# Kernel optimization log

Measured on AMD Instinct MI355X. Metric: run time of the kernel, lower is better.

Reference implementation:

```python
import jax, jax.numpy as jnp
import numpy as np

N, E = 50000, 400000
IN_DIM, EDGE_F, OUT_DIM, EDGE_OUT, H = 256, 64, 32, 64, 8
ALPHA, TEMP, EPS = 0.2, 1.0, 1e-5


def lrelu(x):
    return jax.nn.leaky_relu(x, negative_slope=ALPHA)


def batch_norm(x, gamma, beta):
    # torch BatchNorm1d training-mode: biased variance over the batch dim
    mu = x.mean(0)
    var = x.var(0)
    return (x - mu) * jax.lax.rsqrt(var + EPS) * gamma + beta


def setup_inputs() -> dict:
    key = jax.random.key(0)
    ks = jax.random.split(key, 16)
    s = 0.05
    return {
        "node_inputs": jax.random.normal(ks[0], (N, IN_DIM), jnp.float32),
        "edge_inputs": jax.random.normal(ks[1], (E, EDGE_F), jnp.float32),
        "fc_w": jax.random.normal(ks[2], (IN_DIM, H * OUT_DIM), jnp.float32) * s,
        "attn_l": jax.random.normal(ks[3], (H, OUT_DIM), jnp.float32) * s,
        "attn_r": jax.random.normal(ks[4], (H, OUT_DIM), jnp.float32) * s,
        "ae_w1": jax.random.normal(ks[5], (EDGE_F, OUT_DIM), jnp.float32) * s,
        "ae_b1": jnp.zeros((OUT_DIM,), jnp.float32),
        "ae_w2": jax.random.normal(ks[6], (OUT_DIM, H), jnp.float32) * s,
        "ae_b2": jnp.zeros((H,), jnp.float32),
        "bn_n_g": jnp.ones((H * OUT_DIM,), jnp.float32),
        "bn_n_b": jnp.zeros((H * OUT_DIM,), jnp.float32),
        "eu_node_w": jax.random.normal(ks[7], (2 * H * OUT_DIM, EDGE_OUT), jnp.float32) * s,
        "eu_edge_w": jax.random.normal(ks[8], (EDGE_F, EDGE_OUT), jnp.float32) * s,
        "eu_final_w": jax.random.normal(ks[9], (2 * EDGE_OUT, EDGE_OUT), jnp.float32) * s,
        "bn_e_g": jnp.ones((EDGE_OUT,), jnp.float32),
        "bn_e_b": jnp.zeros((EDGE_OUT,), jnp.float32),
        "src": jax.random.randint(ks[10], (E,), 0, N, jnp.int32),
        "dst": jax.random.randint(ks[11], (E,), 0, N, jnp.int32),
    }


def reference(node_inputs, edge_inputs, fc_w, attn_l, attn_r, ae_w1, ae_b1, ae_w2,
              ae_b2, bn_n_g, bn_n_b, eu_node_w, eu_edge_w, eu_final_w, bn_e_g,
              bn_e_b, src, dst):
    # node projection, per-head attention scalars (dropout prob = 0 -> identity)
    ft = (node_inputs @ fc_w).reshape(N, H, OUT_DIM)          # [N,H,D]
    a1 = jnp.einsum('nhd,hd->nh', ft, attn_l)                 # [N,H]
    a2 = jnp.einsum('nhd,hd->nh', ft, attn_r)                 # [N,H]
    # edge-feature attention MLP: Linear -> LeakyReLU -> Linear
    e_attn = lrelu(edge_inputs @ ae_w1 + ae_b1) @ ae_w2 + ae_b2  # [E,H]
    a = lrelu(a1[src] + a2[dst] + e_attn) * TEMP              # [E,H]
    # two-pass edge softmax over incoming edges (segment by dst)
    a_max = jax.ops.segment_max(a, dst, num_segments=N)       # [N,H]
    a = jnp.exp(a - a_max[dst])                               # [E,H]
    z = jax.ops.segment_sum(a, dst, num_segments=N)           # [N,H]
    # weighted message aggregation
    msg = ft[src] * a[:, :, None]                             # [E,H,D]
    agg = jax.ops.segment_sum(msg, dst, num_segments=N)       # [N,H,D]
    z_safe = jnp.where(z == 0, 1.0, z)
    node_out = (agg / z_safe[:, :, None]).reshape(N, H * OUT_DIM)
    node_out = node_out + node_inputs                         # residual (dims match)
    node_out = batch_norm(lrelu(node_out), bn_n_g, bn_n_b)
    # edge update MLP
    node_f = lrelu(jnp.concatenate([node_out[src], node_out[dst]], -1) @ eu_node_w)
    edge_f = lrelu(edge_inputs @ eu_edge_w)
    edge_out = jnp.concatenate([node_f, edge_f], -1) @ eu_final_w
    edge_out = edge_out + edge_inputs                         # residual (dims match)
    edge_out = batch_norm(lrelu(edge_out), bn_e_g, bn_e_b)
    return node_out, edge_out
```

## Files before the change

kernel.cpp:

```cpp
#include <hip/hip_runtime.h>
#include <hip/hip_bf16.h>

typedef __hip_bfloat16 bf16;

#define N_NODES 50000
#define N_EDGES 400000
#define IN_DIM  256
#define EDGE_F  64
#define OUT_DIM 32
#define EDGE_OUT 64
#define NHEADS  8
#define HD      256
#define ALPHA   0.2f
#define BN_EPS  1e-5f

#define NBINS 50432
#define NBLK  197

__device__ __forceinline__ float b2f(bf16 v){ return __bfloat162float(v); }
__device__ __forceinline__ bf16  f2b(float v){ return __float2bfloat16(v); }
__device__ __forceinline__ float lrelu(float x){ return x > 0.f ? x : ALPHA*x; }
__device__ __forceinline__ unsigned fenc(float f){ unsigned u=__float_as_uint(f); return (u&0x80000000u)? ~u : (u|0x80000000u); }
__device__ __forceinline__ float fdec(unsigned k){ return (k&0x80000000u)? __uint_as_float(k&0x7fffffffu) : __uint_as_float(~k); }

template<bool F32> __device__ __forceinline__ float LD(const void* p, long i){
  if constexpr (F32) return ((const float*)p)[i];
  else               return b2f(((const bf16*)p)[i]);
}
template<bool F32> __device__ __forceinline__ void ST(void* p, long i, float v){
  if constexpr (F32) ((float*)p)[i] = v;
  else               ((bf16*)p)[i] = f2b(v);
}
template<bool F32> __device__ __forceinline__ void* ESEC(void* out){
  return (char*)out + (size_t)N_NODES*HD*(F32?4:2);
}

typedef __attribute__((ext_vector_type(8))) short bf16x8;
typedef __attribute__((ext_vector_type(4))) float f32x4;

union PackU { uint4 u; bf16x8 v; };
__device__ __forceinline__ bf16x8 as_frag(uint4 w){ PackU p; p.u = w; return p.v; }
__device__ __forceinline__ bf16x8 zero_frag(){ PackU p; p.u = make_uint4(0,0,0,0); return p.v; }

#define MFMA16(a,b,c) __builtin_amdgcn_mfma_f32_16x16x32_bf16(a,b,c,0,0,0)

__device__ __forceinline__ void split8(float4 a, float4 b, bf16x8& hi, bf16x8& lo){
  float v[8] = {a.x,a.y,a.z,a.w,b.x,b.y,b.z,b.w};
  unsigned hu[4], lu[4];
  #pragma unroll
  for(int i=0;i<4;i++){
    unsigned u0 = __float_as_uint(v[2*i]);
    unsigned u1 = __float_as_uint(v[2*i+1]);
    unsigned h0 = u0 & 0xffff0000u, h1 = u1 & 0xffff0000u;
    hu[i] = (u0>>16) | h1;
    float l0 = v[2*i]   - __uint_as_float(h0);
    float l1 = v[2*i+1] - __uint_as_float(h1);
    union { bf16 h; unsigned short s; } c0, c1; c0.h = f2b(l0); c1.h = f2b(l1);
    lu[i] = (unsigned)c0.s | ((unsigned)c1.s << 16);
  }
  PackU H,L;
  H.u = make_uint4(hu[0],hu[1],hu[2],hu[3]);
  L.u = make_uint4(lu[0],lu[1],lu[2],lu[3]);
  hi = H.v; lo = L.v;
}

template<bool F32> __device__ __forceinline__ void load_split(const void* p, long off, bf16x8& hi, bf16x8& lo){
  if constexpr(F32){
    const float* f = (const float*)p + off;
    float4 a = *(const float4*)f;
    float4 b = *(const float4*)(f+4);
    split8(a,b,hi,lo);
  } else {
    hi = as_frag(*(const uint4*)((const bf16*)p + off));
    lo = zero_frag();
  }
}

__global__ __launch_bounds__(256) void k_detect(const unsigned short* __restrict__ u,
                                                int* __restrict__ flag){
  __shared__ int cnt;
  if(threadIdx.x==0) cnt=0;
  __syncthreads();
  int local=0;
  for(int i=threadIdx.x;i<8192;i+=256){
    int e = (u[i]>>7)&0xFF;
    if(e>=200) local++;
  }
  atomicAdd(&cnt, local);
  __syncthreads();
  if(threadIdx.x==0) *flag = (cnt>64) ? 1 : 0;
}

__global__ __launch_bounds__(256) void k_hist(const int* __restrict__ dst, int* __restrict__ cnt){
  int e = blockIdx.x*256 + threadIdx.x;
  if(e < N_EDGES){
    unsigned d = (unsigned)dst[e];
    if(d < N_NODES) atomicAdd(&cnt[d], 1);
  }
}
__global__ __launch_bounds__(256) void k_scan1(const int* __restrict__ cnt, int* __restrict__ rs,
                                               int* __restrict__ btot){
  __shared__ int s[256];
  int t = threadIdx.x; int i = blockIdx.x*256 + t;
  int v = cnt[i]; s[t] = v; __syncthreads();
  for(int off=1; off<256; off<<=1){
    int x = (t>=off) ? s[t-off] : 0; __syncthreads();
    s[t] += x; __syncthreads();
  }
  rs[i] = s[t] - v;
  if(t==255) btot[blockIdx.x] = s[t];
}
__global__ __launch_bounds__(256) void k_scan2(const int* __restrict__ btot, int* __restrict__ bsum){
  __shared__ int s[256];
  int t = threadIdx.x;
  int v = (t<NBLK) ? btot[t] : 0; s[t] = v; __syncthreads();
  for(int off=1; off<256; off<<=1){
    int x = (t>=off) ? s[t-off] : 0; __syncthreads();
    s[t] += x; __syncthreads();
  }
  if(t<NBLK) bsum[t] = s[t] - v;
}
__global__ __launch_bounds__(256) void k_scan3(int* __restrict__ rs, const int* __restrict__ bsum,
                                               int* __restrict__ cursor){
  int i = blockIdx.x*256 + threadIdx.x;
  int r = rs[i] + bsum[blockIdx.x];
  rs[i] = r; cursor[i] = r;
}

template<bool F32> __device__ void pack_body(const void* wn, const void* we, const void* wf,
                                             unsigned short* out){
  int i = blockIdx.x*256 + threadIdx.x;
  if(i >= 45056) return;
  const void* srcp; int idx;
  if(i < 32768){ srcp = wn; idx = i; }
  else if(i < 36864){ srcp = we; idx = i - 32768; }
  else { srcp = wf; idx = i - 36864; }
  int j = idx & 7, lane = (idx>>3)&63, nt = (idx>>9)&3, ks = idx>>11;
  int k = ks*32 + ((lane>>4)<<3) + j;
  int n = (nt<<4) + (lane&15);
  union { bf16 h; unsigned short s; } u;
  u.h = f2b(LD<F32>(srcp, (long)k*EDGE_OUT + n));
  out[i] = u.s;
}
__global__ __launch_bounds__(256) void k_pack_w(const void* wn, const void* we, const void* wf,
                                                unsigned short* out, const int* flag){
  if(*flag) pack_body<true >(wn,we,wf,out);
  else      pack_body<false>(wn,we,wf,out);
}
template<bool F32> __device__ void pack_fc_body(const void* w, unsigned short* out){
  int i = blockIdx.x*256 + threadIdx.x;
  int j = i&7, lane = (i>>3)&63, nt = (i>>9)&15, ks = i>>13;
  int k = ks*32 + ((lane>>4)<<3) + j;
  int n = (nt<<4) + (lane&15);
  union { bf16 h; unsigned short s; } u;
  u.h = f2b(LD<F32>(w, (long)k*HD + n));
  out[i] = u.s;
}
__global__ __launch_bounds__(256) void k_pack_fc(const void* w, unsigned short* out, const int* flag){
  if(*flag) pack_fc_body<true >(w,out);
  else      pack_fc_body<false>(w,out);
}

template<bool F32> __device__ void nproj_body(const void* x, const unsigned short* wpf, float* ft){
  const uint4* w4 = (const uint4*)wpf;
  int wid = threadIdx.x>>6, lane = threadIdx.x&63;
  int row16 = lane&15, kgrp = lane>>4;
  int r0 = blockIdx.x*64 + wid*16;
  long arow = r0 + row16; if(arow >= N_NODES) arow = N_NODES-1;
  f32x4 acc[16];
  #pragma unroll
  for(int nt=0;nt<16;nt++) acc[nt] = (f32x4){0.f,0.f,0.f,0.f};
  #pragma unroll 2
  for(int ks=0;ks<8;ks++){
    bf16x8 ah, al;
    load_split<F32>(x, arow*IN_DIM + ks*32 + kgrp*8, ah, al);
    const uint4* wb = w4 + (size_t)(ks*16)*64 + lane;
    #pragma unroll
    for(int nt=0;nt<16;nt++){
      bf16x8 b = as_frag(wb[nt*64]);
      if constexpr(F32) acc[nt] = MFMA16(al, b, acc[nt]);
      acc[nt] = MFMA16(ah, b, acc[nt]);
    }
  }
  #pragma unroll
  for(int nt=0;nt<16;nt++)
    #pragma unroll
    for(int j=0;j<4;j++){
      int r = r0 + kgrp*4 + j;
      if(r < N_NODES) ft[(long)r*HD + nt*16 + row16] = acc[nt][j];
    }
}
__global__ __launch_bounds__(256) void k_node_proj(const void* x, const unsigned short* wpf,
                                                   float* ft, const int* flag){
  if(*flag) nproj_body<true >(x,wpf,ft);
  else      nproj_body<false>(x,wpf,ft);
}

template<bool F32> __device__ void attn_body(const float* ft, const void* al, const void* ar,
                                             float* a1, float* a2){
  int gid = blockIdx.x*8 + (threadIdx.x>>5);
  int d   = threadIdx.x & 31;
  int h   = gid & 7;
  float v  = ft[(long)gid*OUT_DIM + d];
  float s1 = v * LD<F32>(al, h*OUT_DIM + d);
  float s2 = v * LD<F32>(ar, h*OUT_DIM + d);
  for(int o=16;o>0;o>>=1){ s1 += __shfl_down(s1,o,32); s2 += __shfl_down(s2,o,32); }
  if(d==0){ a1[gid]=s1; a2[gid]=s2; }
}
__global__ __launch_bounds__(256) void k_attn(const float* ft, const void* al, const void* ar,
                                              float* a1, float* a2, const int* flag){
  if(*flag) attn_body<true >(ft,al,ar,a1,a2);
  else      attn_body<false>(ft,al,ar,a1,a2);
}

template<bool F32> __device__ void edge_attn_body(const void* ein, const void* w1, const void* b1,
                                                  const void* w2, const void* b2,
                                                  const float* a1, const float* a2,
                                                  const int* src, const int* dst,
                                                  int* cursor, unsigned short* psrc,
                                                  float* a_edge, unsigned* amax, float* sm){
  float* sw1 = sm;
  float* sw2 = sw1 + 2048;
  float* sb1 = sw2 + 256;
  float* sb2 = sb1 + 32;
  float* se  = sb2 + 8;
  float* st  = se  + 512;
  int t = threadIdx.x;
  #pragma unroll
  for(int i=0;i<8;i++) sw1[i*256+t] = LD<F32>(w1, i*256+t);
  sw2[t] = LD<F32>(w2, t);
  if(t<OUT_DIM) sb1[t]=LD<F32>(b1,t);
  if(t<NHEADS)  sb2[t]=LD<F32>(b2,t);
  int e0 = blockIdx.x*8;
  #pragma unroll
  for(int i=0;i<2;i++){ int idx=i*256+t; se[idx] = LD<F32>(ein,(long)e0*EDGE_F + idx); }
  __syncthreads();
  int r = t>>5, j = t&31;
  float acc = sb1[j];
  #pragma unroll 4
  for(int k=0;k<EDGE_F;k++) acc += se[r*64+k]*sw1[k*OUT_DIM+j];
  st[r*32+j] = lrelu(acc);
  __syncthreads();
  if(t<64){
    int rr = t>>3, h = t&7;
    float s = sb2[h];
    #pragma unroll
    for(int jj=0;jj<OUT_DIM;jj++) s += st[rr*32+jj]*sw2[jj*NHEADS+h];
    int e = e0+rr;
    int sv = src[e], dv = dst[e];
    float av = lrelu(a1[sv*NHEADS+h] + a2[dv*NHEADS+h] + s);
    int pos = 0;
    if(h==0) pos = atomicAdd(&cursor[dv], 1);
    pos = __shfl(pos, rr*8, 64);
    a_edge[(long)pos*NHEADS + h] = av;
    if(h==0) psrc[pos] = (unsigned short)sv;
    atomicMax(&amax[dv*NHEADS+h], fenc(av));
  }
}
__global__ __launch_bounds__(256) void k_edge_attn(const void* ein, const void* w1, const void* b1,
                                                   const void* w2, const void* b2,
                                                   const float* a1, const float* a2,
                                                   const int* src, const int* dst,
                                                   int* cursor, unsigned short* psrc,
                                                   float* a_edge, unsigned* amax, const int* flag){
  extern __shared__ float smemf[];
  if(*flag) edge_attn_body<true >(ein,w1,b1,w2,b2,a1,a2,src,dst,cursor,psrc,a_edge,amax,smemf);
  else      edge_attn_body<false>(ein,w1,b1,w2,b2,a1,a2,src,dst,cursor,psrc,a_edge,amax,smemf);
}

template<bool F32> __device__ void agg_body(const int* rs, const unsigned short* psrc,
                                            const float* a_edge, const unsigned* amax,
                                            const float* ft, const void* xin, void* xout,
                                            double* dstats, double* sm){
  int wid = threadIdx.x>>6, lane = threadIdx.x&63;
  int gw = blockIdx.x*4 + wid, nw = gridDim.x*4;
  int h0 = lane>>5;
  double s4[4]={0,0,0,0}, q4[4]={0,0,0,0};
  for(int n=gw; n<N_NODES; n+=nw){
    int b0 = rs[n], b1 = rs[n+1];
    if(b1 > N_EDGES) b1 = N_EDGES;
    if(b0 > b1) b0 = b1;
    float m = (lane<8) ? fdec(amax[n*NHEADS+lane]) : 0.f;
    float zl = 0.f;
    float acc[4] = {0,0,0,0};
    for(int i=b0;i<b1;++i){
      float av = 0.f;
      if(lane<8){ av = __expf(a_edge[(long)i*NHEADS+lane] - m); zl += av; }
      int sv = psrc[i];
      const float* fr = ft + (long)sv*HD;
      #pragma unroll
      for(int q=0;q<4;q++){
        float a = __shfl(av, h0 + 2*q, 64);
        acc[q] = fmaf(a, fr[lane + 64*q], acc[q]);
      }
    }
    #pragma unroll
    for(int q=0;q<4;q++){
      float z = __shfl(zl, h0 + 2*q, 64);
      float zs = (z==0.f) ? 1.f : z;
      int c = lane + 64*q;
      float xv = lrelu(acc[q]/zs + LD<F32>(xin,(long)n*HD + c));
      ST<F32>(xout,(long)n*HD + c, xv);
      s4[q] += xv; q4[q] += (double)xv*(double)xv;
    }
  }
  double* ls = sm; double* lq = sm + 256;
  for(int w=0;w<4;w++){
    if(wid==w){
      #pragma unroll
      for(int q=0;q<4;q++){
        int c = lane + 64*q;
        if(w==0){ ls[c]=s4[q]; lq[c]=q4[q]; }
        else    { ls[c]+=s4[q]; lq[c]+=q4[q]; }
      }
    }
    __syncthreads();
  }
  int t = threadIdx.x;
  unsafeAtomicAdd(&dstats[t],    ls[t]);
  unsafeAtomicAdd(&dstats[HD+t], lq[t]);
}
__global__ __launch_bounds__(256) void k_agg(const int* rs, const unsigned short* psrc,
                                             const float* a_edge, const unsigned* amax,
                                             const float* ft, const void* xin, void* xout,
                                             double* dstats, const int* flag){
  extern __shared__ double smemd[];
  if(*flag) agg_body<true >(rs,psrc,a_edge,amax,ft,xin,xout,dstats,smemd);
  else      agg_body<false>(rs,psrc,a_edge,amax,ft,xin,xout,dstats,smemd);
}

template<bool F32> __device__ void bn_params_body(const double* dstats, const void* g,
                                                  const void* b, float* scsh, int C, double invM){
  int t = threadIdx.x;
  if(t>=C) return;
  double mu  = dstats[t]*invM;
  double var = dstats[C+t]*invM - mu*mu;
  if(var < 0.0) var = 0.0;
  float sc = LD<F32>(g,t) * rsqrtf((float)var + BN_EPS);
  scsh[t]   = sc;
  scsh[C+t] = LD<F32>(b,t) - (float)mu*sc;
}
__global__ void k_bn_params(const double* dstats, const void* g, const void* b,
                            float* scsh, int C, double invM, const int* flag){
  if(*flag) bn_params_body<true >(dstats,g,b,scsh,C,invM);
  else      bn_params_body<false>(dstats,g,b,scsh,C,invM);
}

template<bool F32> __device__ void node_apply_body(void* x, const float* scsh){
  int t = threadIdx.x;
  float sc = scsh[t], sh = scsh[HD+t];
  for(long i=(long)blockIdx.x*256+t; i<(long)N_NODES*HD; i+=(long)gridDim.x*256){
    ST<F32>(x, i, fmaf(LD<F32>(x,i), sc, sh));
  }
}
__global__ __launch_bounds__(256) void k_node_apply(void* x, const float* scsh, const int* flag){
  if(*flag) node_apply_body<true >(x,scsh);
  else      node_apply_body<false>(x,scsh);
}

template<bool F32> __device__ void pq_body(const void* nodeb, const unsigned short* wpack,
                                           float* P, float* Q){
  const uint4* wn4 = (const uint4*)wpack;
  int wid = threadIdx.x>>6, lane = threadIdx.x&63;
  int row16 = lane&15, kgrp = lane>>4;
  int r0 = blockIdx.x*64 + wid*16;
  long arow = r0 + row16; if(arow >= N_NODES) arow = N_NODES-1;
  f32x4 pacc[4], qacc[4];
  #pragma unroll
  for(int nt=0;nt<4;nt++){ pacc[nt]=(f32x4){0.f,0.f,0.f,0.f}; qacc[nt]=(f32x4){0.f,0.f,0.f,0.f}; }
  #pragma unroll 2
  for(int ks=0;ks<8;ks++){
    bf16x8 ah, al;
    load_split<F32>(nodeb, arow*HD + ks*32 + kgrp*8, ah, al);
    const uint4* wbP = wn4 + (size_t)(ks*4)*64 + lane;
    const uint4* wbQ = wn4 + (size_t)((8+ks)*4)*64 + lane;
    #pragma unroll
    for(int nt=0;nt<4;nt++){
      bf16x8 bP = as_frag(wbP[nt*64]);
      bf16x8 bQ = as_frag(wbQ[nt*64]);
      pacc[nt] = MFMA16(ah, bP, pacc[nt]);
      qacc[nt] = MFMA16(ah, bQ, qacc[nt]);
      if constexpr(F32){
        pacc[nt] = MFMA16(al, bP, pacc[nt]);
        qacc[nt] = MFMA16(al, bQ, qacc[nt]);
      }
    }
  }
  #pragma unroll
  for(int nt=0;nt<4;nt++)
    #pragma unroll
    for(int j=0;j<4;j++){
      int r = r0 + kgrp*4 + j;
      if(r < N_NODES){
        P[(long)r*64 + nt*16 + row16] = pacc[nt][j];
        Q[(long)r*64 + nt*16 + row16] = qacc[nt][j];
      }
    }
}
__global__ __launch_bounds__(256) void k_pq(const void* nodeb, const unsigned short* wpack,
                                            float* P, float* Q, const int* flag){
  if(*flag) pq_body<true >(nodeb,wpack,P,Q);
  else      pq_body<false>(nodeb,wpack,P,Q);
}

#define EF_LROW 68

template<bool F32>
__device__ void edge_update_body(const float* P, const float* Q, const void* edge_in,
                                 const int* src, const int* dst,
                                 const unsigned short* wpack,
                                 void* d_out, float* lds){
  void* edge_x = ESEC<F32>(d_out);
  const uint4* we4 = ((const uint4*)wpack) + 4096;
  const uint4* wf4 = ((const uint4*)wpack) + 4608;
  int wid   = threadIdx.x >> 6;
  int lane  = threadIdx.x & 63;
  int row16 = lane & 15;
  int kgrp  = lane >> 4;
  int e0  = blockIdx.x*64 + wid*16;
  int e_a = e0 + row16;
  int nsrc = src[e_a], ndst = dst[e_a];
  float* myl = lds + wid*(16*EF_LROW);

  f32x4 acc_h[4], acc_l[4];
  #pragma unroll
  for(int t=0;t<4;t++){ acc_h[t]=(f32x4){0.f,0.f,0.f,0.f}; acc_l[t]=(f32x4){0.f,0.f,0.f,0.f}; }

  long ebase = (long)e_a * EDGE_F;
  #pragma unroll
  for(int ks=0; ks<2; ks++){
    bf16x8 ah, al;
    load_split<F32>(edge_in, ebase + ks*32 + kgrp*8, ah, al);
    const uint4* wb = we4 + (size_t)(ks*4)*64 + lane;
    #pragma unroll
    for(int nt=0; nt<4; nt++){
      bf16x8 bfr = as_frag(wb[nt*64]);
      acc_h[nt] = MFMA16(ah, bfr, acc_h[nt]);
      if constexpr(F32) acc_l[nt] = MFMA16(al, bfr, acc_l[nt]);
    }
  }
  #pragma unroll
  for(int nt=0; nt<4; nt++)
    #pragma unroll
    for(int j=0;j<4;j++)
      myl[(kgrp*4+j)*EF_LROW + nt*16 + row16] = lrelu(acc_h[nt][j] + acc_l[nt][j]);

  __syncthreads();

  #pragma unroll
  for(int t=0;t<4;t++){ acc_h[t]=(f32x4){0.f,0.f,0.f,0.f}; acc_l[t]=(f32x4){0.f,0.f,0.f,0.f}; }
  #pragma unroll
  for(int ks=0; ks<2; ks++){
    const float* pp = P + (long)nsrc*64 + ks*32 + kgrp*8;
    const float* qq = Q + (long)ndst*64 + ks*32 + kgrp*8;
    float4 p0 = *(const float4*)pp, p1 = *(const float4*)(pp+4);
    float4 q0 = *(const float4*)qq, q1 = *(const float4*)(qq+4);
    float4 v0, v1;
    v0.x = lrelu(p0.x+q0.x); v0.y = lrelu(p0.y+q0.y);
    v0.z = lrelu(p0.z+q0.z); v0.w = lrelu(p0.w+q0.w);
    v1.x = lrelu(p1.x+q1.x); v1.y = lrelu(p1.y+q1.y);
    v1.z = lrelu(p1.z+q1.z); v1.w = lrelu(p1.w+q1.w);
    bf16x8 ah, al; split8(v0, v1, ah, al);
    const uint4* wb = wf4 + (size_t)(ks*4)*64 + lane;
    #pragma unroll
    for(int nt=0; nt<4; nt++){
      bf16x8 bfr = as_frag(wb[nt*64]);
      acc_h[nt] = MFMA16(ah, bfr, acc_h[nt]);
      acc_l[nt] = MFMA16(al, bfr, acc_l[nt]);
    }
  }
  #pragma unroll
  for(int ks=2; ks<4; ks++){
    const float* ap = myl + row16*EF_LROW + (ks-2)*32 + kgrp*8;
    float4 a0 = *(const float4*)ap;
    float4 a1 = *(const float4*)(ap+4);
    bf16x8 ah, al; split8(a0, a1, ah, al);
    const uint4* wb = wf4 + (size_t)(ks*4)*64 + lane;
    #pragma unroll
    for(int nt=0; nt<4; nt++){
      bf16x8 bfr = as_frag(wb[nt*64]);
      acc_h[nt] = MFMA16(ah, bfr, acc_h[nt]);
      acc_l[nt] = MFMA16(al, bfr, acc_l[nt]);
    }
  }
  #pragma unroll
  for(int nt=0; nt<4; nt++)
    #pragma unroll
    for(int j=0;j<4;j++){
      long e = e0 + kgrp*4 + j;
      int  c = nt*16 + row16;
      float res = LD<F32>(edge_in, e*EDGE_OUT + c);
      ST<F32>(edge_x, e*EDGE_OUT + c, lrelu(acc_h[nt][j] + acc_l[nt][j] + res));
    }
}
__global__ __launch_bounds__(256) void k_edge_update(const float* P, const float* Q,
                                                     const void* edge_in,
                                                     const int* src, const int* dst,
                                                     const unsigned short* wpack,
                                                     void* d_out, const int* flag){
  extern __shared__ float smemf[];
  if(*flag) edge_update_body<true >(P,Q,edge_in,src,dst,wpack,d_out,smemf);
  else      edge_update_body<false>(P,Q,edge_in,src,dst,wpack,d_out,smemf);
}

template<bool F32> __device__ void edge_stats_body(void* d_out, double* dstats, double* sm){
  const void* ex = ESEC<F32>(d_out);
  double* ls = sm; double* lq = sm+256;
  int t = threadIdx.x;
  int c = t & 63, r0 = t >> 6;
  double s=0.0, q=0.0;
  for(long i=(long)(blockIdx.x*4 + r0)*64 + c; i < (long)N_EDGES*EDGE_OUT; i += (long)gridDim.x*4*64){
    float x = LD<F32>(ex, i);
    s += x; q += (double)x*(double)x;
  }
  ls[t]=s; lq[t]=q;
  __syncthreads();
  if(t<64){
    double ss = ls[t]+ls[t+64]+ls[t+128]+ls[t+192];
    double qq = lq[t]+lq[t+64]+lq[t+128]+lq[t+192];
    unsafeAtomicAdd(&dstats[t], ss);
    unsafeAtomicAdd(&dstats[64+t], qq);
  }
}
__global__ __launch_bounds__(256) void k_edge_stats(void* d_out, double* dstats, const int* flag){
  extern __shared__ double smemd[];
  if(*flag) edge_stats_body<true >(d_out,dstats,smemd);
  else      edge_stats_body<false>(d_out,dstats,smemd);
}

template<bool F32> __device__ void edge_apply_body(void* d_out, const float* scsh){
  void* ex = ESEC<F32>(d_out);
  int t = threadIdx.x;
  int c = t & 63;
  float sc = scsh[c], sh = scsh[64+c];
  for(long i=(long)blockIdx.x*256+t; i<(long)N_EDGES*EDGE_OUT; i+=(long)gridDim.x*256){
    ST<F32>(ex, i, fmaf(LD<F32>(ex,i), sc, sh));
  }
}
__global__ __launch_bounds__(256) void k_edge_apply(void* d_out, const float* scsh, const int* flag){
  if(*flag) edge_apply_body<true >(d_out,scsh);
  else      edge_apply_body<false>(d_out,scsh);
}

extern "C" void kernel_launch(void* const* d_in, const int* in_sizes, int n_in,
                              void* d_out, int out_size, void* d_ws, size_t ws_size,
                              hipStream_t stream){
  const void* node_in    = d_in[0];
  const void* edge_in    = d_in[1];
  const void* fc_w       = d_in[2];
  const void* attn_l     = d_in[3];
  const void* attn_r     = d_in[4];
  const void* ae_w1      = d_in[5];
  const void* ae_b1      = d_in[6];
  const void* ae_w2      = d_in[7];
  const void* ae_b2      = d_in[8];
  const void* bn_n_g     = d_in[9];
  const void* bn_n_b     = d_in[10];
  const void* eu_node_w  = d_in[11];
  const void* eu_edge_w  = d_in[12];
  const void* eu_final_w = d_in[13];
  const void* bn_e_g     = d_in[14];
  const void* bn_e_b     = d_in[15];
  const int*  src        = (const int*)d_in[16];
  const int*  dst        = (const int*)d_in[17];

  char* base = (char*)d_ws;
  double*   dstats_n = (double*)base;
  double*   dstats_e = (double*)(base + 4096);
  float*    scsh_n   = (float*)(base + 5120);
  float*    scsh_e   = (float*)(base + 7168);
  int*      flag     = (int*)(base + 7680);
  char*     big      = base + 8192;
  float*    ftb      = (float*)big;
  float*    Pb       = (float*)big;
  float*    Qb       = (float*)(big + 12800000);
  float*    a_edge   = (float*)(big + 51200000);
  float*    a1       = (float*)(big + 64000000);
  float*    a2       = (float*)(big + 65600000);
  unsigned* amax     = (unsigned*)(big + 67200000);
  unsigned short* wpack_eu = (unsigned short*)(big + 68800000);
  unsigned short* wpack_fc = (unsigned short*)(big + 68900000);
  int*      rsb      = (int*)(big + 69040000);
  int*      cursor   = (int*)(big + 69250000);
  int*      btot     = (int*)(big + 69460000);
  int*      bsum     = (int*)(big + 69461024);
  unsigned short* psrc = (unsigned short*)(big + 69470000);

  hipMemsetAsync(dstats_n, 0, 640*sizeof(double), stream);
  hipMemsetAsync(amax, 0, (size_t)N_NODES*NHEADS*sizeof(unsigned), stream);
  hipMemsetAsync(cursor, 0, NBINS*sizeof(int), stream);

  k_detect<<<1, 256, 0, stream>>>((const unsigned short*)node_in, flag);
  k_hist <<<(N_EDGES+255)/256, 256, 0, stream>>>(dst, cursor);
  k_scan1<<<NBLK, 256, 0, stream>>>(cursor, rsb, btot);
  k_scan2<<<1, 256, 0, stream>>>(btot, bsum);
  k_scan3<<<NBLK, 256, 0, stream>>>(rsb, bsum, cursor);
  k_pack_fc<<<256, 256, 0, stream>>>(fc_w, wpack_fc, flag);
  k_pack_w<<<176, 256, 0, stream>>>(eu_node_w, eu_edge_w, eu_final_w, wpack_eu, flag);
  k_node_proj<<<(N_NODES+63)/64, 256, 0, stream>>>(node_in, wpack_fc, ftb, flag);
  k_attn<<<N_NODES*NHEADS/8, 256, 0, stream>>>(ftb, attn_l, attn_r, a1, a2, flag);
  k_edge_attn<<<N_EDGES/8, 256, 12448, stream>>>(edge_in, ae_w1, ae_b1, ae_w2, ae_b2,
                                                 a1, a2, src, dst, cursor, psrc,
                                                 a_edge, amax, flag);
  k_agg<<<960, 256, 4096, stream>>>(rsb, psrc, a_edge, amax, ftb, node_in, d_out,
                                    dstats_n, flag);
  k_bn_params<<<1, 256, 0, stream>>>(dstats_n, bn_n_g, bn_n_b, scsh_n, HD, 1.0/N_NODES, flag);
  k_node_apply<<<2048, 256, 0, stream>>>(d_out, scsh_n, flag);
  k_pq<<<(N_NODES+63)/64, 256, 0, stream>>>(d_out, wpack_eu, Pb, Qb, flag);
  k_edge_update<<<N_EDGES/64, 256, 4*16*EF_LROW*4, stream>>>(Pb, Qb, edge_in, src, dst,
                                                             wpack_eu, d_out, flag);
  k_edge_stats<<<512, 256, 4096, stream>>>(d_out, dstats_e, flag);
  k_bn_params<<<1, 256, 0, stream>>>(dstats_e, bn_e_g, bn_e_b, scsh_e, EDGE_OUT, 1.0/N_EDGES, flag);
  k_edge_apply<<<2048, 256, 0, stream>>>(d_out, scsh_e, flag);
  (void)ws_size; (void)out_size; (void)n_in; (void)in_sizes;
}
```

Measured before the change: 925.8 us.

## Compute edge-attention MLP first layer with MFMA and 64 edges per block

The edge-feature attention MLP's first layer (64->32) now runs on MFMA 16x16 bf16 instructions, using split hi/lo bf16 for fp32 inputs. The ae_w1 weights are pre-packed into MFMA fragment layout inside the existing weight-pack kernel. Each block now handles 64 edges instead of 8, which removes the per-block reload of 2K weights into shared memory and the scalar FMA loop. The second layer is spread across all 64 lanes of each wave using a padded shared tile. This adds bf16-split rounding error and relies on a fixed offset into the packed weight buffer.

```diff
diff --git a/kernel.cpp b/kernel.cpp
--- a/kernel.cpp
+++ b/kernel.cpp
@@ -128,24 +128,33 @@
 }
 
 template<bool F32> __device__ void pack_body(const void* wn, const void* we, const void* wf,
-                                             unsigned short* out){
+                                             const void* aw1, unsigned short* out){
   int i = blockIdx.x*256 + threadIdx.x;
-  if(i >= 45056) return;
-  const void* srcp; int idx;
-  if(i < 32768){ srcp = wn; idx = i; }
-  else if(i < 36864){ srcp = we; idx = i - 32768; }
-  else { srcp = wf; idx = i - 36864; }
-  int j = idx & 7, lane = (idx>>3)&63, nt = (idx>>9)&3, ks = idx>>11;
-  int k = ks*32 + ((lane>>4)<<3) + j;
-  int n = (nt<<4) + (lane&15);
+  if(i >= 47104) return;
   union { bf16 h; unsigned short s; } u;
-  u.h = f2b(LD<F32>(srcp, (long)k*EDGE_OUT + n));
+  if(i < 45056){
+    const void* srcp; int idx;
+    if(i < 32768){ srcp = wn; idx = i; }
+    else if(i < 36864){ srcp = we; idx = i - 32768; }
+    else { srcp = wf; idx = i - 36864; }
+    int j = idx & 7, lane = (idx>>3)&63, nt = (idx>>9)&3, ks = idx>>11;
+    int k = ks*32 + ((lane>>4)<<3) + j;
+    int n = (nt<<4) + (lane&15);
+    u.h = f2b(LD<F32>(srcp, (long)k*EDGE_OUT + n));
+  } else {
+    int idx = i - 45056;
+    int j = idx & 7, lane = (idx>>3)&63, nt = (idx>>9)&1, ks = idx>>10;
+    int k = ks*32 + ((lane>>4)<<3) + j;
+    int n = (nt<<4) + (lane&15);
+    u.h = f2b(LD<F32>(aw1, (long)k*OUT_DIM + n));
+  }
   out[i] = u.s;
 }
 __global__ __launch_bounds__(256) void k_pack_w(const void* wn, const void* we, const void* wf,
-                                                unsigned short* out, const int* flag){
-  if(*flag) pack_body<true >(wn,we,wf,out);
-  else      pack_body<false>(wn,we,wf,out);
+                                                const void* aw1, unsigned short* out,
+                                                const int* flag){
+  if(*flag) pack_body<true >(wn,we,wf,aw1,out);
+  else      pack_body<false>(wn,we,wf,aw1,out);
 }
 template<bool F32> __device__ void pack_fc_body(const void* w, unsigned short* out){
   int i = blockIdx.x*256 + threadIdx.x;
@@ -213,59 +222,96 @@
   else      attn_body<false>(ft,al,ar,a1,a2);
 }
 
-template<bool F32> __device__ void edge_attn_body(const void* ein, const void* w1, const void* b1,
-                                                  const void* w2, const void* b2,
-                                                  const float* a1, const float* a2,
-                                                  const int* src, const int* dst,
-                                                  int* cursor, unsigned short* psrc,
-                                                  float* a_edge, unsigned* amax, float* sm){
-  float* sw1 = sm;
-  float* sw2 = sw1 + 2048;
-  float* sb1 = sw2 + 256;
-  float* sb2 = sb1 + 32;
-  float* se  = sb2 + 8;
-  float* st  = se  + 512;
+#define ST_STRIDE 20
+
+template<bool F32>
+__device__ void edge_attn_body(const void* ein, const void* b1, const void* w2, const void* b2,
+                               const float* a1, const float* a2,
+                               const int* src, const int* dst,
+                               int* cursor, unsigned short* psrc,
+                               float* a_edge, unsigned* amax,
+                               const unsigned short* wpack, float* sm){
+  const uint4* aw1 = ((const uint4*)wpack) + 5632;
+  float* sw2f = sm;
+  float* sb1  = sm + 256;
+  float* sb2  = sm + 288;
+  float* st   = sm + 296;
   int t = threadIdx.x;
-  #pragma unroll
-  for(int i=0;i<8;i++) sw1[i*256+t] = LD<F32>(w1, i*256+t);
-  sw2[t] = LD<F32>(w2, t);
-  if(t<OUT_DIM) sb1[t]=LD<F32>(b1,t);
-  if(t<NHEADS)  sb2[t]=LD<F32>(b2,t);
-  int e0 = blockIdx.x*8;
-  #pragma unroll
-  for(int i=0;i<2;i++){ int idx=i*256+t; se[idx] = LD<F32>(ein,(long)e0*EDGE_F + idx); }
+  sw2f[t] = LD<F32>(w2, t);
+  if(t<OUT_DIM) sb1[t] = LD<F32>(b1, t);
+  if(t<NHEADS)  sb2[t] = LD<F32>(b2, t);
   __syncthreads();
-  int r = t>>5, j = t&31;
-  float acc = sb1[j];
-  #pragma unroll 4
-  for(int k=0;k<EDGE_F;k++) acc += se[r*64+k]*sw1[k*OUT_DIM+j];
-  st[r*32+j] = lrelu(acc);
+
+  int wid = t>>6, lane = t&63;
+  int row16 = lane&15, kgrp = lane>>4;
+  int e0w = blockIdx.x*64 + wid*16;
+  int e_a = e0w + row16;
+  float* myst = st + wid*(32*ST_STRIDE);
+
+  f32x4 acc_h[2], acc_l[2];
+  #pragma unroll
+  for(int q=0;q<2;q++){ acc_h[q]=(f32x4){0.f,0.f,0.f,0.f}; acc_l[q]=(f32x4){0.f,0.f,0.f,0.f}; }
+  long ebase = (long)e_a * EDGE_F;
+  #pragma unroll
+  for(int ks=0; ks<2; ks++){
+    bf16x8 ah, al;
+    load_split<F32>(ein, ebase + ks*32 + kgrp*8, ah, al);
+    const uint4* wb = aw1 + (size_t)(ks*2)*64 + lane;
+    #pragma unroll
+    for(int nt=0; nt<2; nt++){
+      bf16x8 bfr = as_frag(wb[nt*64]);
+      acc_h[nt] = MFMA16(ah, bfr, acc_h[nt]);
+      if constexpr(F32) acc_l[nt] = MFMA16(al, bfr, acc_l[nt]);
+    }
+  }
+  #pragma unroll
+  for(int nt=0; nt<2; nt++){
+    int col = nt*16 + row16;
+    float4 v;
+    v.x = lrelu(acc_h[nt][0] + acc_l[nt][0] + sb1[col]);
+    v.y = lrelu(acc_h[nt][1] + acc_l[nt][1] + sb1[col]);
+    v.z = lrelu(acc_h[nt][2] + acc_l[nt][2] + sb1[col]);
+    v.w = lrelu(acc_h[nt][3] + acc_l[nt][3] + sb1[col]);
+    *(float4*)&myst[col*ST_STRIDE + kgrp*4] = v;
+  }
   __syncthreads();
-  if(t<64){
-    int rr = t>>3, h = t&7;
-    float s = sb2[h];
-    #pragma unroll
-    for(int jj=0;jj<OUT_DIM;jj++) s += st[rr*32+jj]*sw2[jj*NHEADS+h];
-    int e = e0+rr;
-    int sv = src[e], dv = dst[e];
-    float av = lrelu(a1[sv*NHEADS+h] + a2[dv*NHEADS+h] + s);
-    int pos = 0;
-    if(h==0) pos = atomicAdd(&cursor[dv], 1);
-    pos = __shfl(pos, rr*8, 64);
-    a_edge[(long)pos*NHEADS + h] = av;
-    if(h==0) psrc[pos] = (unsigned short)sv;
-    atomicMax(&amax[dv*NHEADS+h], fenc(av));
-  }
-}
-__global__ __launch_bounds__(256) void k_edge_attn(const void* ein, const void* w1, const void* b1,
+
+  int h = lane&7, r = lane>>3;
+  float s0 = sb2[h], s1 = sb2[h];
+  #pragma unroll 8
+  for(int k=0;k<OUT_DIM;k++){
+    float w = sw2f[k*NHEADS+h];
+    s0 = fmaf(myst[k*ST_STRIDE + r],     w, s0);
+    s1 = fmaf(myst[k*ST_STRIDE + r + 8], w, s1);
+  }
+  int ea0 = e0w + r, ea1 = e0w + r + 8;
+  int sv0 = src[ea0], dv0 = dst[ea0];
+  int sv1 = src[ea1], dv1 = dst[ea1];
+  float av0 = lrelu(a1[sv0*NHEADS+h] + a2[dv0*NHEADS+h] + s0);
+  float av1 = lrelu(a1[sv1*NHEADS+h] + a2[dv1*NHEADS+h] + s1);
+  int pos0 = 0, pos1 = 0;
+  if(h==0){
+    pos0 = atomicAdd(&cursor[dv0], 1);
+    pos1 = atomicAdd(&cursor[dv1], 1);
+  }
+  pos0 = __shfl(pos0, lane & 56, 64);
+  pos1 = __shfl(pos1, lane & 56, 64);
+  a_edge[(long)pos0*NHEADS + h] = av0;
+  a_edge[(long)pos1*NHEADS + h] = av1;
+  if(h==0){ psrc[pos0] = (unsigned short)sv0; psrc[pos1] = (unsigned short)sv1; }
+  atomicMax(&amax[dv0*NHEADS+h], fenc(av0));
+  atomicMax(&amax[dv1*NHEADS+h], fenc(av1));
+}
+__global__ __launch_bounds__(256) void k_edge_attn(const void* ein, const void* b1,
                                                    const void* w2, const void* b2,
                                                    const float* a1, const float* a2,
                                                    const int* src, const int* dst,
                                                    int* cursor, unsigned short* psrc,
-                                                   float* a_edge, unsigned* amax, const int* flag){
+                                                   float* a_edge, unsigned* amax,
+                                                   const unsigned short* wpack, const int* flag){
   extern __shared__ float smemf[];
-  if(*flag) edge_attn_body<true >(ein,w1,b1,w2,b2,a1,a2,src,dst,cursor,psrc,a_edge,amax,smemf);
-  else      edge_attn_body<false>(ein,w1,b1,w2,b2,a1,a2,src,dst,cursor,psrc,a_edge,amax,smemf);
+  if(*flag) edge_attn_body<true >(ein,b1,w2,b2,a1,a2,src,dst,cursor,psrc,a_edge,amax,wpack,smemf);
+  else      edge_attn_body<false>(ein,b1,w2,b2,a1,a2,src,dst,cursor,psrc,a_edge,amax,wpack,smemf);
 }
 
 template<bool F32> __device__ void agg_body(const int* rs, const unsigned short* psrc,
@@ -596,12 +642,12 @@
   k_scan2<<<1, 256, 0, stream>>>(btot, bsum);
   k_scan3<<<NBLK, 256, 0, stream>>>(rsb, bsum, cursor);
   k_pack_fc<<<256, 256, 0, stream>>>(fc_w, wpack_fc, flag);
-  k_pack_w<<<176, 256, 0, stream>>>(eu_node_w, eu_edge_w, eu_final_w, wpack_eu, flag);
+  k_pack_w<<<184, 256, 0, stream>>>(eu_node_w, eu_edge_w, eu_final_w, ae_w1, wpack_eu, flag);
   k_node_proj<<<(N_NODES+63)/64, 256, 0, stream>>>(node_in, wpack_fc, ftb, flag);
   k_attn<<<N_NODES*NHEADS/8, 256, 0, stream>>>(ftb, attn_l, attn_r, a1, a2, flag);
-  k_edge_attn<<<N_EDGES/8, 256, 12448, stream>>>(edge_in, ae_w1, ae_b1, ae_w2, ae_b2,
-                                                 a1, a2, src, dst, cursor, psrc,
-                                                 a_edge, amax, flag);
+  k_edge_attn<<<N_EDGES/64, 256, (296 + 4*32*ST_STRIDE)*4, stream>>>(
+      edge_in, ae_b1, ae_w2, ae_b2, a1, a2, src, dst, cursor, psrc,
+      a_edge, amax, wpack_eu, flag);
   k_agg<<<960, 256, 4096, stream>>>(rsb, psrc, a_edge, amax, ftb, node_in, d_out,
                                     dstats_n, flag);
   k_bn_params<<<1, 256, 0, stream>>>(dstats_n, bn_n_g, bn_n_b, scsh_n, HD, 1.0/N_NODES, flag);
```

After: 826.6 us. 1.12x faster.
